# Kernel optimization log

Hardware: AMD Instinct MI355X
Metric: run time of the kernel (lower is better)

Reference implementation:

```python
import jax, jax.numpy as jnp
import numpy as np

DIM = 256
B, N, K = 4, 5000, 32


def setup_inputs() -> dict:
    key = jax.random.key(0)
    k1, k2, k3, k4, k5, k6 = jax.random.split(key, 6)
    f_i_set = jax.random.normal(k1, (B, N, DIM), dtype=jnp.float32)
    f_j_set_k = jax.random.normal(k2, (B, N, DIM, K), dtype=jnp.float32)
    # Conv1d(in=1, out=dim, kernel=dim) over a length-dim signal == dense [dim, dim] matmul + bias
    scale = 1.0 / np.sqrt(DIM)
    W1 = jax.random.uniform(k3, (DIM, DIM), jnp.float32, -scale, scale)
    b1 = jax.random.uniform(k4, (DIM,), jnp.float32, -scale, scale)
    W2 = jax.random.uniform(k5, (DIM, DIM), jnp.float32, -scale, scale)
    b2 = jax.random.uniform(k6, (DIM,), jnp.float32, -scale, scale)
    return {"f_i_set": f_i_set, "f_j_set_k": f_j_set_k, "W1": W1, "b1": b1, "W2": W2, "b2": b2}


def reference(f_i_set, f_j_set_k, W1, b1, W2, b2):
    # v_f_i = conv1(f_i): [B, N, DIM]
    v_i = jnp.einsum("bnd,od->bno", f_i_set, W1) + b1
    # edge diff f_j - f_i for each of k neighbors: [B, N, DIM, K]
    diff = f_j_set_k - f_i_set[..., None]
    # v_f_j_i = conv2(f_j - f_i): [B, N, K, DIM]
    v_ji = jnp.einsum("bndk,od->bnko", diff, W2) + b2
    # ReLU then max over k neighbors -> [B, N, DIM]
    feat = jax.nn.relu(v_i[:, :, None, :] + v_ji)
    return jnp.max(feat, axis=2)
```

## Files before the change

### kernel.cpp

```cpp
#include <hip/hip_runtime.h>
#include <hip/hip_bf16.h>

#define DIM 256
#define KNB 32
#define NSITES 20000
#define LDA 264

typedef __attribute__((ext_vector_type(8))) __bf16 bf16x8;
typedef __attribute__((ext_vector_type(4))) float floatx4;
typedef __attribute__((ext_vector_type(4))) unsigned short ushortx4;

union F8 { bf16x8 v; unsigned short u[8]; };

__device__ __forceinline__ unsigned short f2bf(float x) {
    unsigned u = __builtin_bit_cast(unsigned, x);
    u += 0x7fffu + ((u >> 16) & 1u);
    return (unsigned short)(u >> 16);
}

__global__ __launch_bounds__(256, 2) void v3_kernel(
    const float* __restrict__ fi, const float* __restrict__ w1,
    const float* __restrict__ b1, const float* __restrict__ w2,
    const float* __restrict__ b2, float* __restrict__ out)
{
    const int tid  = threadIdx.x;
    const int w    = tid >> 6, lane = tid & 63;
    const int col  = lane & 15, quad = lane >> 4;
    const int sbase = blockIdx.x * 64;

    F8 w3f[4][8];
    float bias[4];
#pragma unroll
    for (int ot = 0; ot < 4; ++ot) {
        const int o = (4 * w + ot) * 16 + col;
        bias[ot] = b1[o] + b2[o];
        const float* p1 = w1 + o * DIM;
        const float* p2 = w2 + o * DIM;
#pragma unroll
        for (int c = 0; c < 8; ++c) {
            const int d0 = c * 32 + quad * 8;
            floatx4 a0 = *(const floatx4*)(p1 + d0);
            floatx4 a1 = *(const floatx4*)(p1 + d0 + 4);
            floatx4 s0 = *(const floatx4*)(p2 + d0);
            floatx4 s1 = *(const floatx4*)(p2 + d0 + 4);
#pragma unroll
            for (int j = 0; j < 4; ++j) {
                w3f[ot][c].u[j]     = f2bf(a0[j] - s0[j]);
                w3f[ot][c].u[j + 4] = f2bf(a1[j] - s1[j]);
            }
        }
    }

#pragma unroll 1
    for (int mt = 0; mt < 4; ++mt) {
        const int srow = sbase + mt * 16;
        if (srow >= NSITES) break;
        F8 a[8];
        const float* pa = fi + (size_t)(srow + col) * DIM;
#pragma unroll
        for (int c = 0; c < 8; ++c) {
            const int d0 = c * 32 + quad * 8;
            floatx4 f0 = *(const floatx4*)(pa + d0);
            floatx4 f1 = *(const floatx4*)(pa + d0 + 4);
#pragma unroll
            for (int j = 0; j < 4; ++j) {
                a[c].u[j]     = f2bf(f0[j]);
                a[c].u[j + 4] = f2bf(f1[j]);
            }
        }
#pragma unroll
        for (int ot = 0; ot < 4; ++ot) {
            floatx4 acc = {0.f, 0.f, 0.f, 0.f};
#pragma unroll
            for (int c = 0; c < 8; ++c)
                acc = __builtin_amdgcn_mfma_f32_16x16x32_bf16(a[c].v, w3f[ot][c].v, acc, 0, 0, 0);
            const int o = (4 * w + ot) * 16 + col;
#pragma unroll
            for (int r = 0; r < 4; ++r) {
                const int site = srow + quad * 4 + r;
                out[(size_t)site * DIM + o] = acc[r] + bias[ot];
            }
        }
    }
}

__global__ __launch_bounds__(512, 2) void edge_kernel(
    const float* __restrict__ fj, const float* __restrict__ w2,
    float* __restrict__ out)
{
    __shared__ unsigned short As[2][KNB * LDA];

    const int tid  = threadIdx.x;
    const int w    = tid >> 6, lane = tid & 63;
    const int col  = lane & 15, quad = lane >> 4;
    const int kg = tid & 7, dg = tid >> 3, db = dg * 4;

    F8 w2f[2][8];
#pragma unroll
    for (int ot = 0; ot < 2; ++ot) {
        const int o = 32 * w + ot * 16 + col;
        const float* p = w2 + o * DIM;
#pragma unroll
        for (int c = 0; c < 8; ++c) {
            const int d0 = c * 32 + quad * 8;
            floatx4 f0 = *(const floatx4*)(p + d0);
            floatx4 f1 = *(const floatx4*)(p + d0 + 4);
#pragma unroll
            for (int j = 0; j < 4; ++j) {
                w2f[ot][c].u[j]     = f2bf(f0[j]);
                w2f[ot][c].u[j + 4] = f2bf(f1[j]);
            }
        }
    }

    const int G = gridDim.x;
    floatx4 r[4];
    auto load_r = [&](int ss) {
        const float* p = fj + (size_t)ss * (DIM * KNB) + (db * KNB + kg * 4);
#pragma unroll
        for (int j = 0; j < 4; ++j)
            r[j] = *(const floatx4*)(p + j * KNB);
    };

    int s = blockIdx.x;
    load_r(s);
    int buf = 0;
    for (;;) {
#pragma unroll
        for (int kk = 0; kk < 4; ++kk) {
            ushortx4 v;
#pragma unroll
            for (int j = 0; j < 4; ++j) v[j] = f2bf(r[j][kk]);
            *(ushortx4*)&As[buf][(4 * kg + kk) * LDA + db] = v;
        }
        __syncthreads();

        const int sn = s + G;
        if (sn < NSITES) load_r(sn);
        const int oidx = s * DIM + 32 * w + (lane & 31);
        float v3 = 0.f;
        if (lane < 32) v3 = out[oidx];

        floatx4 acc[2][2];
#pragma unroll
        for (int mt = 0; mt < 2; ++mt)
#pragma unroll
            for (int ot = 0; ot < 2; ++ot) acc[mt][ot] = (floatx4){0.f, 0.f, 0.f, 0.f};

#pragma unroll
        for (int mt = 0; mt < 2; ++mt) {
            F8 a[8];
#pragma unroll
            for (int c = 0; c < 8; ++c)
                a[c].v = *(const bf16x8*)&As[buf][(mt * 16 + col) * LDA + c * 32 + quad * 8];
#pragma unroll
            for (int ot = 0; ot < 2; ++ot)
#pragma unroll
                for (int c = 0; c < 8; ++c)
                    acc[mt][ot] = __builtin_amdgcn_mfma_f32_16x16x32_bf16(
                        a[c].v, w2f[ot][c].v, acc[mt][ot], 0, 0, 0);
        }

        float mv[2];
#pragma unroll
        for (int ot = 0; ot < 2; ++ot) {
            float m = fmaxf(
                fmaxf(fmaxf(acc[0][ot][0], acc[0][ot][1]), fmaxf(acc[0][ot][2], acc[0][ot][3])),
                fmaxf(fmaxf(acc[1][ot][0], acc[1][ot][1]), fmaxf(acc[1][ot][2], acc[1][ot][3])));
            m = fmaxf(m, __shfl_xor(m, 16));
            m = fmaxf(m, __shfl_xor(m, 32));
            mv[ot] = m;
        }
        if (lane < 32) {
            const float mm = (quad & 1) ? mv[1] : mv[0];
            out[oidx] = fmaxf(v3 + mm, 0.f);
        }

        if (sn >= NSITES) break;
        s = sn; buf ^= 1;
    }
}

extern "C" void kernel_launch(void* const* d_in, const int* in_sizes, int n_in,
                              void* d_out, int out_size, void* d_ws, size_t ws_size,
                              hipStream_t stream) {
    const float* fi = (const float*)d_in[0];
    const float* fj = (const float*)d_in[1];
    const float* w1 = (const float*)d_in[2];
    const float* b1 = (const float*)d_in[3];
    const float* w2 = (const float*)d_in[4];
    const float* b2 = (const float*)d_in[5];
    float* out = (float*)d_out;

    v3_kernel<<<(NSITES + 63) / 64, 256, 0, stream>>>(fi, w1, b1, w2, b2, out);
    edge_kernel<<<256, 512, 0, stream>>>(fj, w2, out);
}
```

Measured before the change: 895.4 us.

## Rebalance edge kernel to 256 threads with 4 output tiles per wave

The edge kernel now runs 256 threads per block with 512 blocks instead of 512 threads with 256 blocks. Each wave holds four output tiles of W2 in registers and each thread loads eight rows of neighbour features, so every shared-memory A fragment feeds four MFMAs instead of two. The v3 intermediate goes to the workspace buffer when one is available, so all 64 lanes can read and write output without aliasing. Register pressure rises sharply (w2f doubles to 4x8 bf16x8 fragments, plus 8 float4 prefetch registers), which risks spills or lower occupancy.

```diff
diff --git a/kernel.cpp b/kernel.cpp
--- a/kernel.cpp
+++ b/kernel.cpp
@@ -21,7 +21,7 @@
 __global__ __launch_bounds__(256, 2) void v3_kernel(
     const float* __restrict__ fi, const float* __restrict__ w1,
     const float* __restrict__ b1, const float* __restrict__ w2,
-    const float* __restrict__ b2, float* __restrict__ out)
+    const float* __restrict__ b2, float* __restrict__ v3out)
 {
     const int tid  = threadIdx.x;
     const int w    = tid >> 6, lane = tid & 63;
@@ -78,27 +78,28 @@
 #pragma unroll
             for (int r = 0; r < 4; ++r) {
                 const int site = srow + quad * 4 + r;
-                out[(size_t)site * DIM + o] = acc[r] + bias[ot];
-            }
-        }
-    }
-}
-
-__global__ __launch_bounds__(512, 2) void edge_kernel(
+                v3out[(size_t)site * DIM + o] = acc[r] + bias[ot];
+            }
+        }
+    }
+}
+
+__global__ __launch_bounds__(256, 2) void edge_kernel(
     const float* __restrict__ fj, const float* __restrict__ w2,
-    float* __restrict__ out)
+    const float* __restrict__ v3buf, float* __restrict__ out)
 {
     __shared__ unsigned short As[2][KNB * LDA];
 
     const int tid  = threadIdx.x;
     const int w    = tid >> 6, lane = tid & 63;
     const int col  = lane & 15, quad = lane >> 4;
-    const int kg = tid & 7, dg = tid >> 3, db = dg * 4;
-
-    F8 w2f[2][8];
-#pragma unroll
-    for (int ot = 0; ot < 2; ++ot) {
-        const int o = 32 * w + ot * 16 + col;
+    const int kg = tid & 7, dg = tid >> 3;
+    const int db = dg * 8;
+
+    F8 w2f[4][8];
+#pragma unroll
+    for (int ot = 0; ot < 4; ++ot) {
+        const int o = 64 * w + ot * 16 + col;
         const float* p = w2 + o * DIM;
 #pragma unroll
         for (int c = 0; c < 8; ++c) {
@@ -114,11 +115,11 @@
     }
 
     const int G = gridDim.x;
-    floatx4 r[4];
+    floatx4 r[8];
     auto load_r = [&](int ss) {
         const float* p = fj + (size_t)ss * (DIM * KNB) + (db * KNB + kg * 4);
 #pragma unroll
-        for (int j = 0; j < 4; ++j)
+        for (int j = 0; j < 8; ++j)
             r[j] = *(const floatx4*)(p + j * KNB);
     };
 
@@ -128,42 +129,47 @@
     for (;;) {
 #pragma unroll
         for (int kk = 0; kk < 4; ++kk) {
-            ushortx4 v;
-#pragma unroll
-            for (int j = 0; j < 4; ++j) v[j] = f2bf(r[j][kk]);
-            *(ushortx4*)&As[buf][(4 * kg + kk) * LDA + db] = v;
+            F8 v;
+#pragma unroll
+            for (int j = 0; j < 8; ++j) v.u[j] = f2bf(r[j][kk]);
+            *(bf16x8*)&As[buf][(4 * kg + kk) * LDA + db] = v.v;
         }
         __syncthreads();
 
         const int sn = s + G;
         if (sn < NSITES) load_r(sn);
-        const int oidx = s * DIM + 32 * w + (lane & 31);
-        float v3 = 0.f;
-        if (lane < 32) v3 = out[oidx];
-
-        floatx4 acc[2][2];
+
+        const int oidx = s * DIM + 64 * w + lane;
+        const float v3 = v3buf[oidx];
+
+        floatx4 acc[2][4];
 #pragma unroll
         for (int mt = 0; mt < 2; ++mt)
 #pragma unroll
-            for (int ot = 0; ot < 2; ++ot) acc[mt][ot] = (floatx4){0.f, 0.f, 0.f, 0.f};
+            for (int ot = 0; ot < 4; ++ot) acc[mt][ot] = (floatx4){0.f, 0.f, 0.f, 0.f};
 
 #pragma unroll
         for (int mt = 0; mt < 2; ++mt) {
-            F8 a[8];
-#pragma unroll
-            for (int c = 0; c < 8; ++c)
-                a[c].v = *(const bf16x8*)&As[buf][(mt * 16 + col) * LDA + c * 32 + quad * 8];
-#pragma unroll
-            for (int ot = 0; ot < 2; ++ot)
-#pragma unroll
-                for (int c = 0; c < 8; ++c)
-                    acc[mt][ot] = __builtin_amdgcn_mfma_f32_16x16x32_bf16(
-                        a[c].v, w2f[ot][c].v, acc[mt][ot], 0, 0, 0);
-        }
-
-        float mv[2];
-#pragma unroll
-        for (int ot = 0; ot < 2; ++ot) {
+            const unsigned short* arow = &As[buf][(mt * 16 + col) * LDA + quad * 8];
+#pragma unroll
+            for (int ch = 0; ch < 2; ++ch) {
+                bf16x8 a0 = *(const bf16x8*)(arow + (ch * 4 + 0) * 32);
+                bf16x8 a1 = *(const bf16x8*)(arow + (ch * 4 + 1) * 32);
+                bf16x8 a2 = *(const bf16x8*)(arow + (ch * 4 + 2) * 32);
+                bf16x8 a3 = *(const bf16x8*)(arow + (ch * 4 + 3) * 32);
+#pragma unroll
+                for (int ot = 0; ot < 4; ++ot) {
+                    acc[mt][ot] = __builtin_amdgcn_mfma_f32_16x16x32_bf16(a0, w2f[ot][ch * 4 + 0].v, acc[mt][ot], 0, 0, 0);
+                    acc[mt][ot] = __builtin_amdgcn_mfma_f32_16x16x32_bf16(a1, w2f[ot][ch * 4 + 1].v, acc[mt][ot], 0, 0, 0);
+                    acc[mt][ot] = __builtin_amdgcn_mfma_f32_16x16x32_bf16(a2, w2f[ot][ch * 4 + 2].v, acc[mt][ot], 0, 0, 0);
+                    acc[mt][ot] = __builtin_amdgcn_mfma_f32_16x16x32_bf16(a3, w2f[ot][ch * 4 + 3].v, acc[mt][ot], 0, 0, 0);
+                }
+            }
+        }
+
+        float mv[4];
+#pragma unroll
+        for (int ot = 0; ot < 4; ++ot) {
             float m = fmaxf(
                 fmaxf(fmaxf(acc[0][ot][0], acc[0][ot][1]), fmaxf(acc[0][ot][2], acc[0][ot][3])),
                 fmaxf(fmaxf(acc[1][ot][0], acc[1][ot][1]), fmaxf(acc[1][ot][2], acc[1][ot][3])));
@@ -171,10 +177,10 @@
             m = fmaxf(m, __shfl_xor(m, 32));
             mv[ot] = m;
         }
-        if (lane < 32) {
-            const float mm = (quad & 1) ? mv[1] : mv[0];
-            out[oidx] = fmaxf(v3 + mm, 0.f);
-        }
+        const float mlo = (quad & 1) ? mv[1] : mv[0];
+        const float mhi = (quad & 1) ? mv[3] : mv[2];
+        const float mm  = (quad & 2) ? mhi : mlo;
+        out[oidx] = fmaxf(v3 + mm, 0.f);
 
         if (sn >= NSITES) break;
         s = sn; buf ^= 1;
@@ -192,6 +198,8 @@
     const float* b2 = (const float*)d_in[5];
     float* out = (float*)d_out;
 
-    v3_kernel<<<(NSITES + 63) / 64, 256, 0, stream>>>(fi, w1, b1, w2, b2, out);
-    edge_kernel<<<256, 512, 0, stream>>>(fj, w2, out);
-}
+    float* v3buf = (ws_size >= (size_t)NSITES * DIM * sizeof(float)) ? (float*)d_ws : out;
+
+    v3_kernel<<<(NSITES + 63) / 64, 256, 0, stream>>>(fi, w1, b1, w2, b2, v3buf);
+    edge_kernel<<<512, 256, 0, stream>>>(fj, w2, v3buf, out);
+}
```

Measured after the change: 899.3 us. Within noise of the previous version (+0.4%).
